# Kernel optimization log

Hardware: AMD Instinct MI355X
Metric: run time of the kernel (lower is better)

Reference implementation:

```python
import jax, jax.numpy as jnp
import numpy as np

N, E, IN_DIM, OUT_DIM, R = 100000, 1600000, 128, 128, 8


def setup_inputs() -> dict:
    key = jax.random.key(0)
    k = jax.random.split(key, 6)
    scale_rel = np.sqrt(6.0 / (IN_DIM + OUT_DIM))  # xavier_uniform bound
    x = jax.random.normal(k[0], (N, IN_DIM), dtype=jnp.float32)
    edge_index = jax.random.randint(k[1], (2, E), 0, N, dtype=jnp.int64)
    edge_type = jax.random.randint(k[2], (E,), 0, R, dtype=jnp.int64)
    rel_weight = jax.random.uniform(k[3], (R, IN_DIM, OUT_DIM), dtype=jnp.float32,
                                    minval=-scale_rel, maxval=scale_rel)
    w_self = jax.random.uniform(k[4], (IN_DIM, OUT_DIM), dtype=jnp.float32,
                                minval=-scale_rel, maxval=scale_rel)
    b_self = jax.random.normal(k[5], (OUT_DIM,), dtype=jnp.float32) * 0.01
    return {"x": x, "edge_index": edge_index, "edge_type": edge_type,
            "rel_weight": rel_weight, "w_self": w_self, "b_self": b_self}


def reference(x, edge_index, edge_type, rel_weight, w_self, b_self):
    n = x.shape[0]
    src, dst = edge_index[0], edge_index[1]
    # self-loop term: W_self @ h_v + b
    out = x @ w_self + b_self                                  # (N, out)
    # pre-transform every node by every relation, then gather per edge.
    # equivalent to per-relation masked (x[src_r] @ W_r) + scatter_add.
    xw = jnp.einsum('ni,rio->nro', x, rel_weight)               # (N, R, out)
    msg = xw[src, edge_type]                                    # (E, out)
    agg = jax.ops.segment_sum(msg, dst, num_segments=n)         # (N, out)
    deg = jax.ops.segment_sum(jnp.ones(dst.shape[0], x.dtype), dst, num_segments=n)
    deg = jnp.clip(deg, 1.0)[:, None]                           # (N, 1)
    return jax.nn.relu(out + agg / deg)
```

## Files before the change

kernel.cpp:

```cpp
#include <hip/hip_runtime.h>
#include <hip/hip_bf16.h>

typedef __attribute__((ext_vector_type(4))) float f32x4_t;
typedef __attribute__((ext_vector_type(8))) short bf16x8_t;

#define NCLS 8

__device__ __forceinline__ float bf2f(ushort u) {
  return __uint_as_float(((unsigned)u) << 16);
}
__device__ __forceinline__ ushort f2bf(float f) {
  unsigned u = __float_as_uint(f);
  u += 0x7fffu + ((u >> 16) & 1u);
  return (ushort)(u >> 16);
}
__device__ __forceinline__ uint packbf2(float x, float y) {
  return (uint)f2bf(x) | ((uint)f2bf(y) << 16);
}

__global__ void deg2_kernel(const int* __restrict__ dst, int* __restrict__ deg2,
                            int N, long E) {
  long i = (long)blockIdx.x * blockDim.x + threadIdx.x;
  long st = (long)gridDim.x * blockDim.x;
  for (; i < E; i += st) {
    int cls = (int)((i >> 8) & (NCLS - 1));
    atomicAdd(&deg2[(size_t)cls * N + dst[i]], 1);
  }
}

__global__ __launch_bounds__(256) void scan1(const int* __restrict__ deg, int* __restrict__ starts,
                                             int* __restrict__ bsum, int M) {
  __shared__ int lds[256];
  const int tid = threadIdx.x;
  const int base = blockIdx.x * 1024 + tid * 4;
  int v0 = 0, v1 = 0, v2 = 0, v3 = 0;
  if (base + 3 < M) {
    int4 q = *(const int4*)(deg + base);
    v0 = q.x; v1 = q.y; v2 = q.z; v3 = q.w;
  } else {
    if (base + 0 < M) v0 = deg[base];
    if (base + 1 < M) v1 = deg[base + 1];
    if (base + 2 < M) v2 = deg[base + 2];
    if (base + 3 < M) v3 = deg[base + 3];
  }
  int s = v0 + v1 + v2 + v3;
  lds[tid] = s;
  __syncthreads();
  for (int off = 1; off < 256; off <<= 1) {
    int t = (tid >= off) ? lds[tid - off] : 0;
    __syncthreads();
    lds[tid] += t;
    __syncthreads();
  }
  int p = lds[tid] - s;
  if (tid == 255) bsum[blockIdx.x] = lds[255];
  if (base + 0 < M) starts[base + 0] = p; p += v0;
  if (base + 1 < M) starts[base + 1] = p; p += v1;
  if (base + 2 < M) starts[base + 2] = p; p += v2;
  if (base + 3 < M) starts[base + 3] = p;
}

__global__ __launch_bounds__(256) void scan2(int* __restrict__ bsum, int nb) {
  __shared__ int lds[256];
  const int tid = threadIdx.x;
  const int base = tid * 4;
  int v[4];
#pragma unroll
  for (int j = 0; j < 4; j++) v[j] = (base + j < nb) ? bsum[base + j] : 0;
  int s = v[0] + v[1] + v[2] + v[3];
  lds[tid] = s;
  __syncthreads();
  for (int off = 1; off < 256; off <<= 1) {
    int t = (tid >= off) ? lds[tid - off] : 0;
    __syncthreads();
    lds[tid] += t;
    __syncthreads();
  }
  int p = lds[tid] - s;
#pragma unroll
  for (int j = 0; j < 4; j++) {
    if (base + j < nb) bsum[base + j] = p;
    p += v[j];
  }
}

__global__ void scan3(int* __restrict__ starts, int* __restrict__ cursor,
                      const int* __restrict__ bsum, int M) {
  int i = blockIdx.x * 256 + threadIdx.x;
  if (i < M) {
    int v = starts[i] + bsum[i >> 10];
    starts[i] = v;
    cursor[i] = v;
  }
}

__global__ void fill_csr(const int* __restrict__ src, const int* __restrict__ dst,
                         const int* __restrict__ et, int* __restrict__ cursor,
                         uint* __restrict__ packed, int N, long E) {
  long i = (long)blockIdx.x * blockDim.x + threadIdx.x;
  long st = (long)gridDim.x * blockDim.x;
  for (; i < E; i += st) {
    int cls = (int)((i >> 8) & (NCLS - 1));
    int pos = atomicAdd(&cursor[(size_t)cls * N + dst[i]], 1);
    packed[pos] = ((uint)src[i] << 4) | (uint)et[i];
  }
}

__global__ void build_wT(const float* __restrict__ rel, const float* __restrict__ wself,
                         ushort* __restrict__ wT, int R) {
  int id = blockIdx.x * blockDim.x + threadIdx.x;
  int total = (R + 1) * 128 * 128;
  if (id >= total) return;
  int r = id >> 14;
  int rem = id & 16383;
  int o = rem >> 7;
  int i = rem & 127;
  float v = (r < R) ? rel[((size_t)r << 14) + (i << 7) + o] : wself[(i << 7) + o];
  wT[id] = f2bf(v);
}

__global__ void conv_x_kernel(const float* __restrict__ x, ushort* __restrict__ S,
                              long n4, int NR) {
  long i = (long)blockIdx.x * blockDim.x + threadIdx.x;
  long st = (long)gridDim.x * blockDim.x;
  const int rowstride = NR * 128;
  const int selfoff = (NR - 1) * 128;
  for (; i < n4; i += st) {
    long node = i >> 5;
    int w = (int)(i & 31) * 4;
    float4 v = ((const float4*)x)[i];
    ushort4 o;
    o.x = f2bf(v.x); o.y = f2bf(v.y); o.z = f2bf(v.z); o.w = f2bf(v.w);
    *(ushort4*)(S + (size_t)node * rowstride + selfoff + w) = o;
  }
}

__global__ __launch_bounds__(256) void gather_sum(const uint* __restrict__ packed,
                                                  const int* __restrict__ starts2,
                                                  const int* __restrict__ deg2,
                                                  ushort* __restrict__ S,
                                                  int N, int NR) {
  const int lane = threadIdx.x & 63;
  const int d = blockIdx.x * 4 + (threadIdx.x >> 6);
  if (d >= N) return;
  const int rowstride = NR * 128;
  const size_t selfoff = (size_t)(NR - 1) * 128;

  int s0[NCLS], ln[NCLS];
#pragma unroll
  for (int c = 0; c < NCLS; c++) s0[c] = starts2[c * N + d];
#pragma unroll
  for (int c = 0; c < NCLS; c++) ln[c] = deg2[c * N + d];

  float a0x = 0, a0y = 0, a1x = 0, a1y = 0, a2x = 0, a2y = 0, a3x = 0, a3y = 0;
  float a4x = 0, a4y = 0, a5x = 0, a5y = 0, a6x = 0, a6y = 0, a7x = 0, a7y = 0;

#define ACCUM(t, vx, vy)                                  \
  switch (t) {                                            \
    case 0: a0x += vx; a0y += vy; break;                  \
    case 1: a1x += vx; a1y += vy; break;                  \
    case 2: a2x += vx; a2y += vy; break;                  \
    case 3: a3x += vx; a3y += vy; break;                  \
    case 4: a4x += vx; a4y += vy; break;                  \
    case 5: a5x += vx; a5y += vy; break;                  \
    case 6: a6x += vx; a6y += vy; break;                  \
    default: a7x += vx; a7y += vy; break;                 \
  }

  int dg = 0;
#pragma unroll 1
  for (int c = 0; c < NCLS; c++) {
    int e = s0[c];
    const int e1 = e + ln[c];
    dg += ln[c];
    for (; e + 1 < e1; e += 2) {
      uint r0 = packed[e], r1 = packed[e + 1];
      ushort2 m0 = *(const ushort2*)(S + (size_t)(r0 >> 4) * rowstride + selfoff + lane * 2);
      ushort2 m1 = *(const ushort2*)(S + (size_t)(r1 >> 4) * rowstride + selfoff + lane * 2);
      float x0 = bf2f(m0.x), y0 = bf2f(m0.y);
      float x1 = bf2f(m1.x), y1 = bf2f(m1.y);
      int t0 = (int)(r0 & 15u), t1 = (int)(r1 & 15u);
      ACCUM(t0, x0, y0);
      ACCUM(t1, x1, y1);
    }
    if (e < e1) {
      uint r0 = packed[e];
      ushort2 m0 = *(const ushort2*)(S + (size_t)(r0 >> 4) * rowstride + selfoff + lane * 2);
      float x0 = bf2f(m0.x), y0 = bf2f(m0.y);
      int t0 = (int)(r0 & 15u);
      ACCUM(t0, x0, y0);
    }
  }
#undef ACCUM

  const float inv = 1.0f / (float)((dg > 1) ? dg : 1);
  uint* Sd = (uint*)(S + (size_t)d * rowstride) + lane;
  __builtin_nontemporal_store(packbf2(a0x * inv, a0y * inv), Sd + 0 * 64);
  __builtin_nontemporal_store(packbf2(a1x * inv, a1y * inv), Sd + 1 * 64);
  __builtin_nontemporal_store(packbf2(a2x * inv, a2y * inv), Sd + 2 * 64);
  __builtin_nontemporal_store(packbf2(a3x * inv, a3y * inv), Sd + 3 * 64);
  __builtin_nontemporal_store(packbf2(a4x * inv, a4y * inv), Sd + 4 * 64);
  __builtin_nontemporal_store(packbf2(a5x * inv, a5y * inv), Sd + 5 * 64);
  __builtin_nontemporal_store(packbf2(a6x * inv, a6y * inv), Sd + 6 * 64);
  __builtin_nontemporal_store(packbf2(a7x * inv, a7y * inv), Sd + 7 * 64);
}

__global__ __launch_bounds__(512) void agg_gemm(const ushort* __restrict__ S,
                                                const ushort* __restrict__ wT,
                                                const float* __restrict__ b,
                                                float* __restrict__ out,
                                                int N, int NR) {
  __shared__ ushort smem[2][16384];

  const int tid = threadIdx.x;
  const int lane = tid & 63;
  const int wave = tid >> 6;
  const int l15 = lane & 15;
  const int l4 = lane >> 4;
  const int nodebase = blockIdx.x * 256 + wave * 32;

  int nd[2], rd[2];
  nd[0] = nodebase + l15;
  nd[1] = nodebase + 16 + l15;
  rd[0] = (nd[0] < N) ? nd[0] : (N - 1);
  rd[1] = (nd[1] < N) ? nd[1] : (N - 1);

  f32x4_t acc[2][8];
#pragma unroll
  for (int g = 0; g < 2; g++)
#pragma unroll
    for (int nt = 0; nt < 8; nt++) acc[g][nt] = {0.f, 0.f, 0.f, 0.f};

  {
    bf16x8_t sreg[4];
#pragma unroll
    for (int j = 0; j < 4; j++) {
      int c = tid + j * 512;
      sreg[j] = *(const bf16x8_t*)(wT + c * 8);
    }
#pragma unroll
    for (int j = 0; j < 4; j++) {
      int c = tid + j * 512;
      int o = c >> 4;
      int colb = (c & 15) * 16;
      int byte = o * 256 + (colb ^ ((o & 7) << 4));
      *(bf16x8_t*)((char*)smem[0] + byte) = sreg[j];
    }
  }
  __syncthreads();

  for (int r = 0; r < NR; r++) {
    bf16x8_t sf[2][4];
#pragma unroll
    for (int g = 0; g < 2; g++) {
      const ushort* srow = S + ((size_t)rd[g] * NR + r) * 128 + l4 * 8;
#pragma unroll
      for (int kk = 0; kk < 4; kk++)
        sf[g][kk] = *(const bf16x8_t*)(srow + kk * 32);
    }

    bf16x8_t sreg[4];
    const bool pf = (r + 1 < NR);
    if (pf) {
      const ushort* wsrc = wT + ((size_t)(r + 1) << 14);
#pragma unroll
      for (int j = 0; j < 4; j++) {
        int c = tid + j * 512;
        sreg[j] = *(const bf16x8_t*)(wsrc + c * 8);
      }
    }

    const char* wbuf = (const char*)smem[r & 1];
#pragma unroll
    for (int nt = 0; nt < 8; nt++) {
      bf16x8_t wf[4];
      const int row = nt * 16 + l15;
      const int swz = (row & 7) << 4;
#pragma unroll
      for (int kk = 0; kk < 4; kk++) {
        int colb = l4 * 16 + kk * 64;
        wf[kk] = *(const bf16x8_t*)(wbuf + row * 256 + (colb ^ swz));
      }
#pragma unroll
      for (int g = 0; g < 2; g++)
#pragma unroll
        for (int kk = 0; kk < 4; kk++)
          acc[g][nt] = __builtin_amdgcn_mfma_f32_16x16x32_bf16(wf[kk], sf[g][kk], acc[g][nt], 0, 0, 0);
    }

    if (pf) {
#pragma unroll
      for (int j = 0; j < 4; j++) {
        int c = tid + j * 512;
        int o = c >> 4;
        int colb = (c & 15) * 16;
        int byte = o * 256 + (colb ^ ((o & 7) << 4));
        *(bf16x8_t*)((char*)smem[(r + 1) & 1] + byte) = sreg[j];
      }
    }
    __syncthreads();
  }

#pragma unroll
  for (int g = 0; g < 2; g++) {
    if (nd[g] < N) {
#pragma unroll
      for (int nt = 0; nt < 8; nt++) {
        float4 bv = *(const float4*)(b + nt * 16 + l4 * 4);
        f32x4_t v = acc[g][nt];
        float4 o;
        o.x = fmaxf(v[0] + bv.x, 0.f);
        o.y = fmaxf(v[1] + bv.y, 0.f);
        o.z = fmaxf(v[2] + bv.z, 0.f);
        o.w = fmaxf(v[3] + bv.w, 0.f);
        *(float4*)(out + (size_t)nd[g] * 128 + nt * 16 + l4 * 4) = o;
      }
    }
  }
}

__global__ void deg_kernel(const int* __restrict__ dst, int* __restrict__ deg, long E) {
  long i = (long)blockIdx.x * blockDim.x + threadIdx.x;
  long st = (long)gridDim.x * blockDim.x;
  for (; i < E; i += st) atomicAdd(&deg[dst[i]], 1);
}
__global__ void naive_edge(const float* __restrict__ x, const int* __restrict__ src,
                           const int* __restrict__ dst, const int* __restrict__ et,
                           const float* __restrict__ rel, float* __restrict__ agg, long E) {
  const int lane = threadIdx.x & 63;
  long wid = ((long)blockIdx.x * blockDim.x + threadIdx.x) >> 6;
  long nw = ((long)gridDim.x * blockDim.x) >> 6;
  for (long e = wid; e < E; e += nw) {
    int s = src[e];
    int d = dst[e];
    int t = et[e];
    const float* xs = x + (size_t)s * 128;
    const float* w = rel + (size_t)t * 128 * 128;
    float a0 = 0.f, a1 = 0.f;
    for (int i = 0; i < 128; i++) {
      float xv = xs[i];
      a0 += xv * w[i * 128 + lane];
      a1 += xv * w[i * 128 + lane + 64];
    }
    atomicAdd(agg + (size_t)d * 128 + lane, a0);
    atomicAdd(agg + (size_t)d * 128 + lane + 64, a1);
  }
}
__global__ void naive_self(const float* __restrict__ x, const float* __restrict__ ws,
                           const float* __restrict__ b, const int* __restrict__ deg,
                           float* __restrict__ out, int N) {
  int v = blockIdx.x;
  int o = threadIdx.x;
  if (v >= N) return;
  const float* xv = x + (size_t)v * 128;
  float acc = b[o];
  for (int i = 0; i < 128; i++) acc += xv[i] * ws[i * 128 + o];
  float dg = (float)max(deg[v], 1);
  float val = acc + out[(size_t)v * 128 + o] / dg;
  out[(size_t)v * 128 + o] = fmaxf(val, 0.f);
}

extern "C" void kernel_launch(void* const* d_in, const int* in_sizes, int n_in,
                              void* d_out, int out_size, void* d_ws, size_t ws_size,
                              hipStream_t stream) {
  const float* x = (const float*)d_in[0];
  const int* ei = (const int*)d_in[1];
  const int* et = (const int*)d_in[2];
  const float* rel = (const float*)d_in[3];
  const float* wself = (const float*)d_in[4];
  const float* bself = (const float*)d_in[5];
  float* out = (float*)d_out;

  const int N = in_sizes[0] / 128;
  const long E = in_sizes[2];
  const int R = in_sizes[3] / (128 * 128);
  const int NR = R + 1;
  const int* srcp = ei;
  const int* dstp = ei + E;
  const int M = NCLS * N;

  size_t off = 0;
  auto alloc = [&](size_t bytes) {
    size_t o = off;
    off += (bytes + 255) & ~(size_t)255;
    return o;
  };
  size_t deg2_off = alloc((size_t)M * 4);
  size_t starts2_off = alloc((size_t)M * 4);
  size_t cursor2_off = alloc((size_t)M * 4);
  size_t bsum_off = alloc(4096);
  size_t wT_off = alloc((size_t)NR * 128 * 128 * 2);
  size_t packed_off = alloc((size_t)E * 4);
  size_t S_off = alloc((size_t)N * (size_t)NR * 128 * 2);
  const bool main_path = (ws_size >= off) && (M <= 1024 * 1024) && (R <= 8);

  if (main_path) {
    int* deg2 = (int*)((char*)d_ws + deg2_off);
    int* starts2 = (int*)((char*)d_ws + starts2_off);
    int* cursor2 = (int*)((char*)d_ws + cursor2_off);
    int* bsum = (int*)((char*)d_ws + bsum_off);
    ushort* wT = (ushort*)((char*)d_ws + wT_off);
    uint* packed = (uint*)((char*)d_ws + packed_off);
    ushort* S = (ushort*)((char*)d_ws + S_off);

    hipMemsetAsync(deg2, 0, (size_t)M * 4, stream);
    deg2_kernel<<<2048, 256, 0, stream>>>(dstp, deg2, N, E);

    const int nb = (M + 1023) / 1024;
    scan1<<<nb, 256, 0, stream>>>(deg2, starts2, bsum, M);
    scan2<<<1, 256, 0, stream>>>(bsum, nb);
    scan3<<<(M + 255) / 256, 256, 0, stream>>>(starts2, cursor2, bsum, M);
    fill_csr<<<2048, 256, 0, stream>>>(srcp, dstp, et, cursor2, packed, N, E);
    conv_x_kernel<<<2048, 256, 0, stream>>>(x, S, (long)N * 32, NR);
    build_wT<<<(NR * 16384 + 255) / 256, 256, 0, stream>>>(rel, wself, wT, R);
    gather_sum<<<(N + 3) / 4, 256, 0, stream>>>(packed, starts2, deg2, S, N, NR);
    agg_gemm<<<(N + 255) / 256, 512, 0, stream>>>(S, wT, bself, out, N, NR);
  } else {
    int* deg = (int*)((char*)d_ws + deg2_off);
    hipMemsetAsync(deg, 0, (size_t)N * 4, stream);
    deg_kernel<<<2048, 256, 0, stream>>>(dstp, deg, E);
    hipMemsetAsync(out, 0, (size_t)out_size * 4, stream);
    naive_edge<<<4096, 256, 0, stream>>>(x, srcp, dstp, et, rel, out, E);
    naive_self<<<N, 128, 0, stream>>>(x, wself, bself, deg, out, N);
  }
}
```

Baseline: 493.9 us.

## Use per-node contiguous CSR and a separate compact bf16 x buffer for gathers

Reorganizes the CSR so each destination node's edges sit in one contiguous range: class offsets are computed per node instead of by an 8x-larger scan over class-major segments. The scan shrinks from 8N to N entries, and gather_sum runs one 4-way unrolled loop instead of eight small segments. Converted x now lives in its own dense 256-byte-row buffer instead of a strided slot inside S, so random gathers touch a compact array with better cache locality. The GEMM reads the self row from that buffer. This adds small nodedeg and cursor_init kernels and restricts the fast path to R==8.

```diff
diff --git a/kernel.cpp b/kernel.cpp
--- a/kernel.cpp
+++ b/kernel.cpp
@@ -26,6 +26,15 @@
     int cls = (int)((i >> 8) & (NCLS - 1));
     atomicAdd(&deg2[(size_t)cls * N + dst[i]], 1);
   }
+}
+
+__global__ void nodedeg_kernel(const int* __restrict__ deg2, int* __restrict__ nodedeg, int N) {
+  int d = blockIdx.x * 256 + threadIdx.x;
+  if (d >= N) return;
+  int s = 0;
+#pragma unroll
+  for (int c = 0; c < NCLS; c++) s += deg2[(size_t)c * N + d];
+  nodedeg[d] = s;
 }
 
 __global__ __launch_bounds__(256) void scan1(const int* __restrict__ deg, int* __restrict__ starts,
@@ -84,13 +93,20 @@
   }
 }
 
-__global__ void scan3(int* __restrict__ starts, int* __restrict__ cursor,
-                      const int* __restrict__ bsum, int M) {
+__global__ void scan3(int* __restrict__ starts, const int* __restrict__ bsum, int M) {
   int i = blockIdx.x * 256 + threadIdx.x;
-  if (i < M) {
-    int v = starts[i] + bsum[i >> 10];
-    starts[i] = v;
-    cursor[i] = v;
+  if (i < M) starts[i] += bsum[i >> 10];
+}
+
+__global__ void cursor_init(const int* __restrict__ deg2, const int* __restrict__ node_starts,
+                            int* __restrict__ cursor, int N) {
+  int d = blockIdx.x * 256 + threadIdx.x;
+  if (d >= N) return;
+  int run = node_starts[d];
+#pragma unroll
+  for (int c = 0; c < NCLS; c++) {
+    cursor[(size_t)c * N + d] = run;
+    run += deg2[(size_t)c * N + d];
   }
 }
 
@@ -119,38 +135,30 @@
   wT[id] = f2bf(v);
 }
 
-__global__ void conv_x_kernel(const float* __restrict__ x, ushort* __restrict__ S,
-                              long n4, int NR) {
+__global__ void conv_x_kernel(const float* __restrict__ x, ushort* __restrict__ xb, long n4) {
   long i = (long)blockIdx.x * blockDim.x + threadIdx.x;
   long st = (long)gridDim.x * blockDim.x;
-  const int rowstride = NR * 128;
-  const int selfoff = (NR - 1) * 128;
   for (; i < n4; i += st) {
-    long node = i >> 5;
-    int w = (int)(i & 31) * 4;
     float4 v = ((const float4*)x)[i];
     ushort4 o;
     o.x = f2bf(v.x); o.y = f2bf(v.y); o.z = f2bf(v.z); o.w = f2bf(v.w);
-    *(ushort4*)(S + (size_t)node * rowstride + selfoff + w) = o;
+    ((ushort4*)xb)[i] = o;
   }
 }
 
 __global__ __launch_bounds__(256) void gather_sum(const uint* __restrict__ packed,
-                                                  const int* __restrict__ starts2,
-                                                  const int* __restrict__ deg2,
+                                                  const int* __restrict__ node_starts,
+                                                  const int* __restrict__ nodedeg,
+                                                  const ushort* __restrict__ xb,
                                                   ushort* __restrict__ S,
-                                                  int N, int NR) {
+                                                  int N) {
   const int lane = threadIdx.x & 63;
   const int d = blockIdx.x * 4 + (threadIdx.x >> 6);
   if (d >= N) return;
-  const int rowstride = NR * 128;
-  const size_t selfoff = (size_t)(NR - 1) * 128;
-
-  int s0[NCLS], ln[NCLS];
-#pragma unroll
-  for (int c = 0; c < NCLS; c++) s0[c] = starts2[c * N + d];
-#pragma unroll
-  for (int c = 0; c < NCLS; c++) ln[c] = deg2[c * N + d];
+
+  const int s0 = node_starts[d];
+  const int dg = nodedeg[d];
+  const int e1 = s0 + dg;
 
   float a0x = 0, a0y = 0, a1x = 0, a1y = 0, a2x = 0, a2y = 0, a3x = 0, a3y = 0;
   float a4x = 0, a4y = 0, a5x = 0, a5y = 0, a6x = 0, a6y = 0, a7x = 0, a7y = 0;
@@ -167,34 +175,30 @@
     default: a7x += vx; a7y += vy; break;                 \
   }
 
-  int dg = 0;
-#pragma unroll 1
-  for (int c = 0; c < NCLS; c++) {
-    int e = s0[c];
-    const int e1 = e + ln[c];
-    dg += ln[c];
-    for (; e + 1 < e1; e += 2) {
-      uint r0 = packed[e], r1 = packed[e + 1];
-      ushort2 m0 = *(const ushort2*)(S + (size_t)(r0 >> 4) * rowstride + selfoff + lane * 2);
-      ushort2 m1 = *(const ushort2*)(S + (size_t)(r1 >> 4) * rowstride + selfoff + lane * 2);
-      float x0 = bf2f(m0.x), y0 = bf2f(m0.y);
-      float x1 = bf2f(m1.x), y1 = bf2f(m1.y);
-      int t0 = (int)(r0 & 15u), t1 = (int)(r1 & 15u);
-      ACCUM(t0, x0, y0);
-      ACCUM(t1, x1, y1);
-    }
-    if (e < e1) {
-      uint r0 = packed[e];
-      ushort2 m0 = *(const ushort2*)(S + (size_t)(r0 >> 4) * rowstride + selfoff + lane * 2);
-      float x0 = bf2f(m0.x), y0 = bf2f(m0.y);
-      int t0 = (int)(r0 & 15u);
-      ACCUM(t0, x0, y0);
-    }
+  int e = s0;
+  for (; e + 3 < e1; e += 4) {
+    uint r0 = packed[e], r1 = packed[e + 1], r2 = packed[e + 2], r3 = packed[e + 3];
+    ushort2 m0 = *(const ushort2*)(xb + (size_t)(r0 >> 4) * 128 + lane * 2);
+    ushort2 m1 = *(const ushort2*)(xb + (size_t)(r1 >> 4) * 128 + lane * 2);
+    ushort2 m2 = *(const ushort2*)(xb + (size_t)(r2 >> 4) * 128 + lane * 2);
+    ushort2 m3 = *(const ushort2*)(xb + (size_t)(r3 >> 4) * 128 + lane * 2);
+    int t0 = (int)(r0 & 15u), t1 = (int)(r1 & 15u);
+    int t2 = (int)(r2 & 15u), t3 = (int)(r3 & 15u);
+    ACCUM(t0, bf2f(m0.x), bf2f(m0.y));
+    ACCUM(t1, bf2f(m1.x), bf2f(m1.y));
+    ACCUM(t2, bf2f(m2.x), bf2f(m2.y));
+    ACCUM(t3, bf2f(m3.x), bf2f(m3.y));
+  }
+  for (; e < e1; e++) {
+    uint r0 = packed[e];
+    ushort2 m0 = *(const ushort2*)(xb + (size_t)(r0 >> 4) * 128 + lane * 2);
+    int t0 = (int)(r0 & 15u);
+    ACCUM(t0, bf2f(m0.x), bf2f(m0.y));
   }
 #undef ACCUM
 
   const float inv = 1.0f / (float)((dg > 1) ? dg : 1);
-  uint* Sd = (uint*)(S + (size_t)d * rowstride) + lane;
+  uint* Sd = (uint*)(S + (size_t)d * 1024) + lane;
   __builtin_nontemporal_store(packbf2(a0x * inv, a0y * inv), Sd + 0 * 64);
   __builtin_nontemporal_store(packbf2(a1x * inv, a1y * inv), Sd + 1 * 64);
   __builtin_nontemporal_store(packbf2(a2x * inv, a2y * inv), Sd + 2 * 64);
@@ -206,6 +210,7 @@
 }
 
 __global__ __launch_bounds__(512) void agg_gemm(const ushort* __restrict__ S,
+                                                const ushort* __restrict__ xb,
                                                 const ushort* __restrict__ wT,
                                                 const float* __restrict__ b,
                                                 float* __restrict__ out,
@@ -253,7 +258,8 @@
     bf16x8_t sf[2][4];
 #pragma unroll
     for (int g = 0; g < 2; g++) {
-      const ushort* srow = S + ((size_t)rd[g] * NR + r) * 128 + l4 * 8;
+      const ushort* srow = (r < NR - 1) ? (S + ((size_t)rd[g] * 8 + r) * 128 + l4 * 8)
+                                        : (xb + (size_t)rd[g] * 128 + l4 * 8);
 #pragma unroll
       for (int kk = 0; kk < 4; kk++)
         sf[g][kk] = *(const bf16x8_t*)(srow + kk * 32);
@@ -377,7 +383,6 @@
   const int NR = R + 1;
   const int* srcp = ei;
   const int* dstp = ei + E;
-  const int M = NCLS * N;
 
   size_t off = 0;
   auto alloc = [&](size_t bytes) {
@@ -385,36 +390,42 @@
     off += (bytes + 255) & ~(size_t)255;
     return o;
   };
-  size_t deg2_off = alloc((size_t)M * 4);
-  size_t starts2_off = alloc((size_t)M * 4);
-  size_t cursor2_off = alloc((size_t)M * 4);
+  size_t deg2_off = alloc((size_t)NCLS * N * 4);
+  size_t nodedeg_off = alloc((size_t)N * 4);
+  size_t nstart_off = alloc((size_t)N * 4);
+  size_t cursor_off = alloc((size_t)NCLS * N * 4);
   size_t bsum_off = alloc(4096);
   size_t wT_off = alloc((size_t)NR * 128 * 128 * 2);
   size_t packed_off = alloc((size_t)E * 4);
-  size_t S_off = alloc((size_t)N * (size_t)NR * 128 * 2);
-  const bool main_path = (ws_size >= off) && (M <= 1024 * 1024) && (R <= 8);
+  size_t xb_off = alloc((size_t)N * 128 * 2);
+  size_t S_off = alloc((size_t)N * 8 * 128 * 2);
+  const bool main_path = (ws_size >= off) && (N <= 1024 * 1024) && (R == 8);
 
   if (main_path) {
     int* deg2 = (int*)((char*)d_ws + deg2_off);
-    int* starts2 = (int*)((char*)d_ws + starts2_off);
-    int* cursor2 = (int*)((char*)d_ws + cursor2_off);
+    int* nodedeg = (int*)((char*)d_ws + nodedeg_off);
+    int* nstart = (int*)((char*)d_ws + nstart_off);
+    int* cursor = (int*)((char*)d_ws + cursor_off);
     int* bsum = (int*)((char*)d_ws + bsum_off);
     ushort* wT = (ushort*)((char*)d_ws + wT_off);
     uint* packed = (uint*)((char*)d_ws + packed_off);
+    ushort* xb = (ushort*)((char*)d_ws + xb_off);
     ushort* S = (ushort*)((char*)d_ws + S_off);
 
-    hipMemsetAsync(deg2, 0, (size_t)M * 4, stream);
+    hipMemsetAsync(deg2, 0, (size_t)NCLS * N * 4, stream);
     deg2_kernel<<<2048, 256, 0, stream>>>(dstp, deg2, N, E);
-
-    const int nb = (M + 1023) / 1024;
-    scan1<<<nb, 256, 0, stream>>>(deg2, starts2, bsum, M);
+    nodedeg_kernel<<<(N + 255) / 256, 256, 0, stream>>>(deg2, nodedeg, N);
+
+    const int nb = (N + 1023) / 1024;
+    scan1<<<nb, 256, 0, stream>>>(nodedeg, nstart, bsum, N);
     scan2<<<1, 256, 0, stream>>>(bsum, nb);
-    scan3<<<(M + 255) / 256, 256, 0, stream>>>(starts2, cursor2, bsum, M);
-    fill_csr<<<2048, 256, 0, stream>>>(srcp, dstp, et, cursor2, packed, N, E);
-    conv_x_kernel<<<2048, 256, 0, stream>>>(x, S, (long)N * 32, NR);
+    scan3<<<(N + 255) / 256, 256, 0, stream>>>(nstart, bsum, N);
+    cursor_init<<<(N + 255) / 256, 256, 0, stream>>>(deg2, nstart, cursor, N);
+    fill_csr<<<2048, 256, 0, stream>>>(srcp, dstp, et, cursor, packed, N, E);
+    conv_x_kernel<<<2048, 256, 0, stream>>>(x, xb, (long)N * 32);
     build_wT<<<(NR * 16384 + 255) / 256, 256, 0, stream>>>(rel, wself, wT, R);
-    gather_sum<<<(N + 3) / 4, 256, 0, stream>>>(packed, starts2, deg2, S, N, NR);
-    agg_gemm<<<(N + 255) / 256, 512, 0, stream>>>(S, wT, bself, out, N, NR);
+    gather_sum<<<(N + 3) / 4, 256, 0, stream>>>(packed, nstart, nodedeg, xb, S, N);
+    agg_gemm<<<(N + 255) / 256, 512, 0, stream>>>(S, xb, wT, bself, out, N, NR);
   } else {
     int* deg = (int*)((char*)d_ws + deg2_off);
     hipMemsetAsync(deg, 0, (size_t)N * 4, stream);
```

After: 463.7 us. -6.1%, faster.
